# Kernel tuning notes

Hardware: AMD Instinct MI355X
Metric: run time of the kernel (lower is better)

## Reference

```python
import jax, jax.numpy as jnp
import numpy as np

D_MODEL = 1024
N_HEAD = 16
D_K = D_MODEL // N_HEAD


def setup_inputs() -> dict:
    key = jax.random.key(0)
    ks = jax.random.split(key, 9)
    s = 1.0 / np.sqrt(D_MODEL)
    return {
        "x": jax.random.normal(ks[0], (2, 2048, D_MODEL), dtype=jnp.float32),
        "Wq": jax.random.uniform(ks[1], (D_MODEL, D_MODEL), jnp.float32, -s, s),
        "bq": jax.random.uniform(ks[2], (D_MODEL,), jnp.float32, -s, s),
        "Wk": jax.random.uniform(ks[3], (D_MODEL, D_MODEL), jnp.float32, -s, s),
        "bk": jax.random.uniform(ks[4], (D_MODEL,), jnp.float32, -s, s),
        "Wv": jax.random.uniform(ks[5], (D_MODEL, D_MODEL), jnp.float32, -s, s),
        "bv": jax.random.uniform(ks[6], (D_MODEL,), jnp.float32, -s, s),
        "Wo": jax.random.uniform(ks[7], (D_MODEL, D_MODEL), jnp.float32, -s, s),
        "bo": jax.random.uniform(ks[8], (D_MODEL,), jnp.float32, -s, s),
    }


def reference(x, Wq, bq, Wk, bk, Wv, bv, Wo, bo):
    B, S, D = x.shape
    # linear projections (torch Linear: x @ W.T + b)
    q = x @ Wq.T + bq
    k = x @ Wk.T + bk
    v = x @ Wv.T + bv
    # split heads: [B, H, S, d_k]
    q = q.reshape(B, S, N_HEAD, D_K).transpose(0, 2, 1, 3)
    k = k.reshape(B, S, N_HEAD, D_K).transpose(0, 2, 1, 3)
    v = v.reshape(B, S, N_HEAD, D_K).transpose(0, 2, 1, 3)
    scores = jnp.einsum("bhqd,bhkd->bhqk", q, k) / np.sqrt(D_K).astype(jnp.float32)
    attn = jax.nn.softmax(scores, axis=-1)
    out = jnp.einsum("bhqk,bhkd->bhqd", attn, v)
    out = out.transpose(0, 2, 1, 3).reshape(B, S, D)
    return out @ Wo.T + bo
```

## Files before the change

kernel.cpp:

```cpp
#include <hip/hip_runtime.h>
#include <hip/hip_bf16.h>


typedef unsigned short u16;
typedef __attribute__((ext_vector_type(4))) unsigned short u16x4;
typedef __attribute__((ext_vector_type(8))) short short8;
typedef __attribute__((ext_vector_type(4))) float f32x4;

__device__ __forceinline__ u16 f2bf(float f) {
  __bf16 b = (__bf16)f;
  return __builtin_bit_cast(unsigned short, b);
}

__device__ __forceinline__ f32x4 mfma_bf16(short8 a, short8 b, f32x4 c) {
  return __builtin_amdgcn_mfma_f32_16x16x32_bf16(a, b, c, 0, 0, 0);
}

#define GLL16(gp, lp) __builtin_amdgcn_global_load_lds( \
    (const __attribute__((address_space(1))) void*)(gp), \
    (__attribute__((address_space(3))) void*)(lp), 16, 0, 0)

#define QSCALE 0.18033688011112042f

__global__ __launch_bounds__(256) void cast_all(
    const float* __restrict__ x,
    const float* __restrict__ wq, const float* __restrict__ wk,
    const float* __restrict__ wv, const float* __restrict__ wo,
    u16* __restrict__ xb, u16* __restrict__ wqb, u16* __restrict__ wkb,
    u16* __restrict__ wvb, u16* __restrict__ wob)
{
  const int z = blockIdx.z;
  const float* s; u16* d; int n4;
  if (z == 0)      { s = x;  d = xb;  n4 = 1048576; }
  else if (z == 1) { s = wq; d = wqb; n4 = 262144; }
  else if (z == 2) { s = wk; d = wkb; n4 = 262144; }
  else if (z == 3) { s = wv; d = wvb; n4 = 262144; }
  else             { s = wo; d = wob; n4 = 262144; }
  int i = blockIdx.x * 256 + threadIdx.x;
  if (i >= n4) return;
  float4 v = ((const float4*)s)[i];
  u16x4 o; o[0] = f2bf(v.x); o[1] = f2bf(v.y); o[2] = f2bf(v.z); o[3] = f2bf(v.w);
  ((u16x4*)d)[i] = o;
}

__global__ __launch_bounds__(512, 2) void gemm_qkv(
    const u16* __restrict__ X, const u16* __restrict__ Wqkv,
    const float* __restrict__ bq, const float* __restrict__ bk, const float* __restrict__ bv,
    u16* __restrict__ Qo, u16* __restrict__ Ko, u16* __restrict__ Vt)
{
  __shared__ u16 smem[65536];
  u16* const sA0 = smem;
  u16* const sA1 = smem + 16384;
  u16* const sB0 = smem + 32768;
  u16* const sB1 = smem + 49152;

  const int tid = threadIdx.x, lane = tid & 63, w = tid >> 6;
  const int wr = w >> 2, wcn = w & 3;
  const int rl = lane & 15, g = lane >> 4, rsw = rl & 7;

  const int bflat = blockIdx.x;
  const int xcd = bflat & 7, idx = bflat >> 3;
  const int mt = xcd * 2 + (idx & 1);
  const int nt = idx >> 1;
  const int m0 = mt * 256;
  const int z = nt >> 2;
  const int colbase = (nt & 3) * 256;

  const int lr = lane >> 3, lc = lane & 7;
  const size_t srcoff = (size_t)(w * 8 + lr) * 1024 + ((lc ^ lr) * 8);
  const u16* gaS = X    + (size_t)m0 * 1024 + srcoff;
  const u16* gbS = Wqkv + (size_t)(nt * 256) * 1024 + srcoff;

  f32x4 acc[8][4];
#pragma unroll
  for (int mf = 0; mf < 8; ++mf)
#pragma unroll
    for (int nf = 0; nf < 4; ++nf) acc[mf][nf] = (f32x4){0.f, 0.f, 0.f, 0.f};

  auto loadA = [&](const u16* buf, int mf, int kh) -> short8 {
    return *(const short8*)&buf[(wr * 128 + mf * 16 + rl) * 64 +
                                (((kh * 4 + g) ^ rsw) * 8)];
  };
  auto loadB = [&](const u16* buf, int nf, int kh) -> short8 {
    return *(const short8*)&buf[(wcn * 64 + nf * 16 + rl) * 64 +
                                (((kh * 4 + g) ^ rsw) * 8)];
  };

  auto proc_tile = [&](const u16* bufA, const u16* bufB,
                       u16* stA, u16* stB, int ts, bool doSt) {
    short8 af[4], bf[4];
    if (doSt) {
#pragma unroll
      for (int i = 0; i < 4; ++i)
        GLL16(gaS + (size_t)(i * 64) * 1024 + ts * 64, stA + (i * 64 + w * 8) * 64);
    }
#pragma unroll
    for (int nf = 0; nf < 4; ++nf) bf[nf] = loadB(bufB, nf, 0);
#pragma unroll
    for (int i = 0; i < 4; ++i) af[i] = loadA(bufA, i, 0);
    __builtin_amdgcn_s_setprio(1);
#pragma unroll
    for (int i = 0; i < 4; ++i)
#pragma unroll
      for (int nf = 0; nf < 4; ++nf)
        acc[i][nf] = mfma_bf16(af[i], bf[nf], acc[i][nf]);
    __builtin_amdgcn_s_setprio(0);
    __builtin_amdgcn_s_barrier();
    if (doSt) {
#pragma unroll
      for (int i = 0; i < 4; ++i)
        GLL16(gbS + (size_t)(i * 64) * 1024 + ts * 64, stB + (i * 64 + w * 8) * 64);
    }
#pragma unroll
    for (int i = 0; i < 4; ++i) af[i] = loadA(bufA, 4 + i, 0);
    __builtin_amdgcn_s_setprio(1);
#pragma unroll
    for (int i = 0; i < 4; ++i)
#pragma unroll
      for (int nf = 0; nf < 4; ++nf)
        acc[4 + i][nf] = mfma_bf16(af[i], bf[nf], acc[4 + i][nf]);
    __builtin_amdgcn_s_setprio(0);
    __builtin_amdgcn_s_barrier();
#pragma unroll
    for (int nf = 0; nf < 4; ++nf) bf[nf] = loadB(bufB, nf, 1);
#pragma unroll
    for (int i = 0; i < 4; ++i) af[i] = loadA(bufA, i, 1);
    __builtin_amdgcn_s_setprio(1);
#pragma unroll
    for (int i = 0; i < 4; ++i)
#pragma unroll
      for (int nf = 0; nf < 4; ++nf)
        acc[i][nf] = mfma_bf16(af[i], bf[nf], acc[i][nf]);
    __builtin_amdgcn_s_setprio(0);
    __builtin_amdgcn_s_barrier();
#pragma unroll
    for (int i = 0; i < 4; ++i) af[i] = loadA(bufA, 4 + i, 1);
    __builtin_amdgcn_s_setprio(1);
#pragma unroll
    for (int i = 0; i < 4; ++i)
#pragma unroll
      for (int nf = 0; nf < 4; ++nf)
        acc[4 + i][nf] = mfma_bf16(af[i], bf[nf], acc[4 + i][nf]);
    __builtin_amdgcn_s_setprio(0);
  };

#pragma unroll
  for (int i = 0; i < 4; ++i) {
    GLL16(gaS + (size_t)(i * 64) * 1024, sA0 + (i * 64 + w * 8) * 64);
    GLL16(gbS + (size_t)(i * 64) * 1024, sB0 + (i * 64 + w * 8) * 64);
  }
  __syncthreads();

#pragma unroll 1
  for (int tt = 0; tt < 8; ++tt) {
    proc_tile(sA0, sB0, sA1, sB1, 2 * tt + 1, true);
    __syncthreads();
    proc_tile(sA1, sB1, sA0, sB0, 2 * tt + 2, tt < 7);
    __syncthreads();
  }

  const int rg = g * 4;
  if (z < 2) {
    u16* dst = (z == 0) ? Qo : Ko;
    const float cs = (z == 0) ? QSCALE : 1.0f;
    const float* bias = (z == 0) ? bq : bk;
#pragma unroll
    for (int nf = 0; nf < 4; ++nf) {
      int col = colbase + wcn * 64 + nf * 16 + rl;
      float bb = bias[col];
#pragma unroll
      for (int mf = 0; mf < 8; ++mf) {
        int row0 = m0 + wr * 128 + mf * 16 + rg;
#pragma unroll
        for (int r = 0; r < 4; ++r)
          dst[(size_t)(row0 + r) * 1024 + col] = f2bf((acc[mf][nf][r] + bb) * cs);
      }
    }
  } else {
#pragma unroll
    for (int nf = 0; nf < 4; ++nf) {
      int col = colbase + wcn * 64 + nf * 16 + rl;
      float bb = bv[col];
#pragma unroll
      for (int mf = 0; mf < 8; ++mf) {
        int row0 = m0 + wr * 128 + mf * 16 + rg;
        int bidx = row0 >> 11, sl = row0 & 2047;
        u16x4 pk;
#pragma unroll
        for (int r = 0; r < 4; ++r) pk[r] = f2bf(acc[mf][nf][r] + bb);
        *(u16x4*)&Vt[((size_t)(bidx * 1024 + col)) * 2048 + sl] = pk;
      }
    }
  }
}

__global__ __launch_bounds__(256) void gemm_out(
    const u16* __restrict__ Ob, const u16* __restrict__ Wob,
    const float* __restrict__ bo, float* __restrict__ Out)
{
  __shared__ u16 sA[2048], sB[4096];
  const int bflat = blockIdx.x;
  const int xcd = bflat & 7, idx = bflat >> 3;
  const int m0 = (xcd * 8 + (idx & 7)) * 64;
  const int n0 = (idx >> 3) * 128;

  const int tid = threadIdx.x, lane = tid & 63, wave = tid >> 6;
  const int wr = wave >> 1, wc = wave & 1;
  const u16* ga = Ob  + (size_t)(m0 + (tid >> 2)) * 1024 + (tid & 3) * 8;
  const u16* gb = Wob + (size_t)(n0 + (tid >> 2)) * 1024 + (tid & 3) * 8;
  u16* la0 = sA + wave * 512;
  u16* lb0 = sB + wave * 512;          u16* lb1 = sB + 2048 + wave * 512;
  const int rl = lane & 15, kg = (lane >> 4) * 8, rg = (lane >> 4) * 4;

  f32x4 acc[2][4];
#pragma unroll
  for (int m = 0; m < 2; ++m)
#pragma unroll
    for (int n = 0; n < 4; ++n) acc[m][n] = (f32x4){0.f, 0.f, 0.f, 0.f};

  for (int k0 = 0; k0 < 1024; k0 += 32) {
    GLL16(ga + k0,             la0);
    GLL16(gb + k0,             lb0);
    GLL16(gb + 64 * 1024 + k0, lb1);
    __syncthreads();
    short8 af[2], bf_[4];
#pragma unroll
    for (int m = 0; m < 2; ++m) af[m]  = *(const short8*)&sA[(wr * 32 + m * 16 + rl) * 32 + kg];
#pragma unroll
    for (int n = 0; n < 4; ++n) bf_[n] = *(const short8*)&sB[(wc * 64 + n * 16 + rl) * 32 + kg];
#pragma unroll
    for (int m = 0; m < 2; ++m)
#pragma unroll
      for (int n = 0; n < 4; ++n)
        acc[m][n] = mfma_bf16(af[m], bf_[n], acc[m][n]);
    __syncthreads();
  }

#pragma unroll
  for (int n = 0; n < 4; ++n) {
    int col = n0 + wc * 64 + n * 16 + rl;
    float bb = bo[col];
#pragma unroll
    for (int m = 0; m < 2; ++m) {
      int row0 = m0 + wr * 32 + m * 16 + rg;
#pragma unroll
      for (int r = 0; r < 4; ++r)
        Out[(size_t)(row0 + r) * 1024 + col] = acc[m][n][r] + bb;
    }
  }
}

__global__ __launch_bounds__(512) void attn_fwd(
    const u16* __restrict__ Q, const u16* __restrict__ K,
    const u16* __restrict__ Vt, u16* __restrict__ O)
{
  __shared__ u16 sK[2][64][64];
  __shared__ u16 sV[2][64][64];

  const int tid = threadIdx.x, lane = tid & 63, wave = tid >> 6;
  const int rl = lane & 15, g = lane >> 4;

  const int bflat = blockIdx.x;
  const int xcd = bflat & 7, j = bflat >> 3;
  const int bh = xcd * 4 + (j >> 4);
  const int qchunk = j & 15;
  const int b = bh >> 4, h = bh & 15;
  const int qbase = qchunk * 128 + wave * 16;

  const u16* Qp = Q + (size_t)(b * 2048 + qbase) * 1024 + h * 64;
  const u16* Kp = K + (size_t)(b * 2048) * 1024 + h * 64;
  const u16* Vp = Vt + (size_t)(bh * 64) * 2048;

  short8 qf[2];
#pragma unroll
  for (int hf = 0; hf < 2; ++hf)
    qf[hf] = *(const short8*)&Qp[(size_t)rl * 1024 + hf * 32 + g * 8];

  const int keyperm = 8 * (rl >> 2) + (rl & 3);
  const int swzK8 = (((rl & 3) | (((rl >> 2) & 1) << 2))) * 8;
  const int swzV8 = (rl & 7) * 8;

  const int srow = lane >> 3;
  const int feK = (((lane & 7) ^ (srow & 3)) * 8) ^ ((wave & 1) * 32);
  const int feV = (((lane & 7) ^ srow) * 8);

  f32x4 oacc[4];
  f32x4 lacc = (f32x4){0.f, 0.f, 0.f, 0.f};
#pragma unroll
  for (int dg = 0; dg < 4; ++dg) oacc[dg] = (f32x4){0.f, 0.f, 0.f, 0.f};
  float mrun = -INFINITY;

  const short8 ONES = {0x3F80, 0x3F80, 0x3F80, 0x3F80,
                       0x3F80, 0x3F80, 0x3F80, 0x3F80};

  auto stage = [&](int nb, int kt) {
    const int grow = wave * 8 + srow;
    GLL16(Kp + (size_t)(kt + grow) * 1024 + feK, &sK[nb][wave * 8][0]);
    GLL16(Vp + (size_t)grow * 2048 + kt + feV,   &sV[nb][wave * 8][0]);
  };

  auto proc_sub = [&](int nb, int sub) {
    short8 kf[2][2];
#pragma unroll
    for (int t = 0; t < 2; ++t) {
      const int r = sub * 32 + keyperm + 4 * t;
#pragma unroll
      for (int hf = 0; hf < 2; ++hf)
        kf[t][hf] = *(const short8*)&sK[nb][r][(hf * 32 + g * 8) ^ swzK8];
    }
    short8 vf[4];
#pragma unroll
    for (int dg = 0; dg < 4; ++dg)
      vf[dg] = *(const short8*)&sV[nb][dg * 16 + rl][(sub * 32 + g * 8) ^ swzV8];

    f32x4 sc[2];
    __builtin_amdgcn_s_setprio(1);
#pragma unroll
    for (int t = 0; t < 2; ++t) {
      f32x4 a = (f32x4){0.f, 0.f, 0.f, 0.f};
      a = mfma_bf16(kf[t][0], qf[0], a);
      a = mfma_bf16(kf[t][1], qf[1], a);
      sc[t] = a;
    }
    __builtin_amdgcn_s_setprio(0);

    float p2[8];
#pragma unroll
    for (int t = 0; t < 2; ++t)
#pragma unroll
      for (int r = 0; r < 4; ++r) p2[t * 4 + r] = sc[t][r];
    float a0 = fmaxf(fmaxf(p2[0], p2[1]), p2[2]);
    float a1 = fmaxf(fmaxf(p2[3], p2[4]), p2[5]);
    float a2 = fmaxf(p2[6], p2[7]);
    float tm = fmaxf(fmaxf(a0, a1), a2);
    if (!__all(tm <= mrun + 8.0f)) {
      tm = fmaxf(tm, __shfl_xor(tm, 16));
      tm = fmaxf(tm, __shfl_xor(tm, 32));
      float mnew = fmaxf(mrun, tm);
      float sfac = __builtin_amdgcn_exp2f(mrun - mnew);
      mrun = mnew;
#pragma unroll
      for (int dg = 0; dg < 4; ++dg)
#pragma unroll
        for (int r = 0; r < 4; ++r) oacc[dg][r] *= sfac;
      lacc[0] *= sfac;
    }
    short8 pb;
#pragma unroll
    for (int j2 = 0; j2 < 8; ++j2)
      pb[j2] = (short)f2bf(__builtin_amdgcn_exp2f(p2[j2] - mrun));

    __builtin_amdgcn_s_setprio(1);
    lacc = mfma_bf16(ONES, pb, lacc);
#pragma unroll
    for (int dg = 0; dg < 4; ++dg)
      oacc[dg] = mfma_bf16(vf[dg], pb, oacc[dg]);
    __builtin_amdgcn_s_setprio(0);
  };

  stage(0, 0);
  __syncthreads();
  for (int kt = 0; kt < 2048; kt += 128) {
    stage(1, kt + 64);
    proc_sub(0, 0);
    proc_sub(0, 1);
    __syncthreads();
    if (kt + 128 < 2048) stage(0, kt + 128);
    proc_sub(1, 0);
    proc_sub(1, 1);
    __syncthreads();
  }

  float inv = 1.0f / lacc[0];
  int qrow = qbase + rl;
  u16* op = O + (size_t)(b * 2048 + qrow) * 1024 + h * 64;
#pragma unroll
  for (int dg = 0; dg < 4; ++dg) {
    u16x4 pk;
#pragma unroll
    for (int r = 0; r < 4; ++r) pk[r] = f2bf(oacc[dg][r] * inv);
    *(u16x4*)&op[dg * 16 + g * 4] = pk;
  }
}

extern "C" void kernel_launch(void* const* d_in, const int* in_sizes, int n_in,
                              void* d_out, int out_size, void* d_ws, size_t ws_size,
                              hipStream_t stream) {
  const float* x  = (const float*)d_in[0];
  const float* Wq = (const float*)d_in[1];
  const float* bq = (const float*)d_in[2];
  const float* Wk = (const float*)d_in[3];
  const float* bk = (const float*)d_in[4];
  const float* Wv = (const float*)d_in[5];
  const float* bv = (const float*)d_in[6];
  const float* Wo = (const float*)d_in[7];
  const float* bo = (const float*)d_in[8];

  char* ws = (char*)d_ws;
  const size_t MB = 1024 * 1024;
  u16* Xb  = (u16*)(ws + 0 * MB);
  u16* Wqb = (u16*)(ws + 8 * MB);
  u16* Wkb = (u16*)(ws + 10 * MB);
  u16* Wvb = (u16*)(ws + 12 * MB);
  u16* Wob = (u16*)(ws + 14 * MB);
  u16* Qb  = (u16*)(ws + 16 * MB);
  u16* Kb  = (u16*)(ws + 24 * MB);
  u16* Vtb = (u16*)(ws + 32 * MB);
  u16* Ob  = (u16*)(ws + 40 * MB);

  cast_all<<<dim3(4096, 1, 5), 256, 0, stream>>>(x, Wq, Wk, Wv, Wo,
                                                 Xb, Wqb, Wkb, Wvb, Wob);
  gemm_qkv<<<dim3(192), 512, 0, stream>>>(Xb, Wqb, bq, bk, bv, Qb, Kb, Vtb);
  attn_fwd<<<dim3(512), 512, 0, stream>>>(Qb, Kb, Vtb, Ob);
  gemm_out<<<dim3(512), 256, 0, stream>>>(Ob, Wob, bo, (float*)d_out);
}
```

Before: 110.5 us.

## Retile output projection to 256x256 double-buffered GEMM and flatten cast grid

The output projection GEMM moves from 64x128 tiles with a single LDS buffer to the 256x256 tile scheme used by the QKV GEMM. That scheme uses 512 threads, a double-buffered XOR-swizzled LDS layout, 64-wide K steps and interleaved prefetch with setprio around the MFMA blocks. The goal is more data reuse per block and hiding global load latency. The trade-off is that only 64 blocks are launched, which may leave many CUs idle on a 256-CU part. The cast kernel also drops the z-dimension grid, which removed the wasted blocks that covered the smaller weight tensors, and now writes the weights as one contiguous panel.

```diff
diff --git a/kernel.cpp b/kernel.cpp
--- a/kernel.cpp
+++ b/kernel.cpp
@@ -26,21 +26,22 @@
     const float* __restrict__ x,
     const float* __restrict__ wq, const float* __restrict__ wk,
     const float* __restrict__ wv, const float* __restrict__ wo,
-    u16* __restrict__ xb, u16* __restrict__ wqb, u16* __restrict__ wkb,
-    u16* __restrict__ wvb, u16* __restrict__ wob)
+    u16* __restrict__ xb, u16* __restrict__ wpanel)
 {
-  const int z = blockIdx.z;
-  const float* s; u16* d; int n4;
-  if (z == 0)      { s = x;  d = xb;  n4 = 1048576; }
-  else if (z == 1) { s = wq; d = wqb; n4 = 262144; }
-  else if (z == 2) { s = wk; d = wkb; n4 = 262144; }
-  else if (z == 3) { s = wv; d = wvb; n4 = 262144; }
-  else             { s = wo; d = wob; n4 = 262144; }
   int i = blockIdx.x * 256 + threadIdx.x;
-  if (i >= n4) return;
+  const float* s; u16x4* d;
+  if (i < 1048576) {
+    s = x; d = (u16x4*)xb + i;
+  } else {
+    int j = i - 1048576;
+    int w = j >> 18;
+    const float* ws4 = (w == 0) ? wq : (w == 1) ? wk : (w == 2) ? wv : wo;
+    s = ws4; d = (u16x4*)wpanel + j;
+    i = j & 262143;
+  }
   float4 v = ((const float4*)s)[i];
   u16x4 o; o[0] = f2bf(v.x); o[1] = f2bf(v.y); o[2] = f2bf(v.z); o[3] = f2bf(v.w);
-  ((u16x4*)d)[i] = o;
+  *d = o;
 }
 
 __global__ __launch_bounds__(512, 2) void gemm_qkv(
@@ -194,58 +195,130 @@
   }
 }
 
-__global__ __launch_bounds__(256) void gemm_out(
+__global__ __launch_bounds__(512, 2) void gemm_out(
     const u16* __restrict__ Ob, const u16* __restrict__ Wob,
     const float* __restrict__ bo, float* __restrict__ Out)
 {
-  __shared__ u16 sA[2048], sB[4096];
+  __shared__ u16 smem[65536];
+  u16* const sA0 = smem;
+  u16* const sA1 = smem + 16384;
+  u16* const sB0 = smem + 32768;
+  u16* const sB1 = smem + 49152;
+
+  const int tid = threadIdx.x, lane = tid & 63, w = tid >> 6;
+  const int wr = w >> 2, wcn = w & 3;
+  const int rl = lane & 15, g = lane >> 4, rsw = rl & 7;
+
   const int bflat = blockIdx.x;
   const int xcd = bflat & 7, idx = bflat >> 3;
-  const int m0 = (xcd * 8 + (idx & 7)) * 64;
-  const int n0 = (idx >> 3) * 128;
-
-  const int tid = threadIdx.x, lane = tid & 63, wave = tid >> 6;
-  const int wr = wave >> 1, wc = wave & 1;
-  const u16* ga = Ob  + (size_t)(m0 + (tid >> 2)) * 1024 + (tid & 3) * 8;
-  const u16* gb = Wob + (size_t)(n0 + (tid >> 2)) * 1024 + (tid & 3) * 8;
-  u16* la0 = sA + wave * 512;
-  u16* lb0 = sB + wave * 512;          u16* lb1 = sB + 2048 + wave * 512;
-  const int rl = lane & 15, kg = (lane >> 4) * 8, rg = (lane >> 4) * 4;
-
-  f32x4 acc[2][4];
-#pragma unroll
-  for (int m = 0; m < 2; ++m)
-#pragma unroll
-    for (int n = 0; n < 4; ++n) acc[m][n] = (f32x4){0.f, 0.f, 0.f, 0.f};
-
-  for (int k0 = 0; k0 < 1024; k0 += 32) {
-    GLL16(ga + k0,             la0);
-    GLL16(gb + k0,             lb0);
-    GLL16(gb + 64 * 1024 + k0, lb1);
-    __syncthreads();
-    short8 af[2], bf_[4];
-#pragma unroll
-    for (int m = 0; m < 2; ++m) af[m]  = *(const short8*)&sA[(wr * 32 + m * 16 + rl) * 32 + kg];
-#pragma unroll
-    for (int n = 0; n < 4; ++n) bf_[n] = *(const short8*)&sB[(wc * 64 + n * 16 + rl) * 32 + kg];
-#pragma unroll
-    for (int m = 0; m < 2; ++m)
-#pragma unroll
-      for (int n = 0; n < 4; ++n)
-        acc[m][n] = mfma_bf16(af[m], bf_[n], acc[m][n]);
-    __syncthreads();
-  }
-
-#pragma unroll
-  for (int n = 0; n < 4; ++n) {
-    int col = n0 + wc * 64 + n * 16 + rl;
+  const int mt = xcd * 2 + (idx & 1);
+  const int nt = idx >> 1;
+  const int m0 = mt * 256;
+
+  const int lr = lane >> 3, lc = lane & 7;
+  const size_t srcoff = (size_t)(w * 8 + lr) * 1024 + ((lc ^ lr) * 8);
+  const u16* gaS = Ob  + (size_t)m0 * 1024 + srcoff;
+  const u16* gbS = Wob + (size_t)(nt * 256) * 1024 + srcoff;
+
+  f32x4 acc[8][4];
+#pragma unroll
+  for (int mf = 0; mf < 8; ++mf)
+#pragma unroll
+    for (int nf = 0; nf < 4; ++nf) acc[mf][nf] = (f32x4){0.f, 0.f, 0.f, 0.f};
+
+  auto loadA = [&](const u16* buf, int mf, int kh) -> short8 {
+    return *(const short8*)&buf[(wr * 128 + mf * 16 + rl) * 64 +
+                                (((kh * 4 + g) ^ rsw) * 8)];
+  };
+  auto loadB = [&](const u16* buf, int nf, int kh) -> short8 {
+    return *(const short8*)&buf[(wcn * 64 + nf * 16 + rl) * 64 +
+                                (((kh * 4 + g) ^ rsw) * 8)];
+  };
+
+  auto proc_tile = [&](const u16* bufA, const u16* bufB,
+                       u16* stA, u16* stB, int ts, bool doSt) {
+    short8 af[4], bf[4];
+    if (doSt) {
+#pragma unroll
+      for (int i = 0; i < 4; ++i)
+        GLL16(gaS + (size_t)(i * 64) * 1024 + ts * 64, stA + (i * 64 + w * 8) * 64);
+    }
+#pragma unroll
+    for (int nf = 0; nf < 4; ++nf) bf[nf] = loadB(bufB, nf, 0);
+#pragma unroll
+    for (int i = 0; i < 4; ++i) af[i] = loadA(bufA, i, 0);
+    __builtin_amdgcn_s_setprio(1);
+#pragma unroll
+    for (int i = 0; i < 4; ++i)
+#pragma unroll
+      for (int nf = 0; nf < 4; ++nf)
+        acc[i][nf] = mfma_bf16(af[i], bf[nf], acc[i][nf]);
+    __builtin_amdgcn_s_setprio(0);
+    __builtin_amdgcn_s_barrier();
+    if (doSt) {
+#pragma unroll
+      for (int i = 0; i < 4; ++i)
+        GLL16(gbS + (size_t)(i * 64) * 1024 + ts * 64, stB + (i * 64 + w * 8) * 64);
+    }
+#pragma unroll
+    for (int i = 0; i < 4; ++i) af[i] = loadA(bufA, 4 + i, 0);
+    __builtin_amdgcn_s_setprio(1);
+#pragma unroll
+    for (int i = 0; i < 4; ++i)
+#pragma unroll
+      for (int nf = 0; nf < 4; ++nf)
+        acc[4 + i][nf] = mfma_bf16(af[i], bf[nf], acc[4 + i][nf]);
+    __builtin_amdgcn_s_setprio(0);
+    __builtin_amdgcn_s_barrier();
+#pragma unroll
+    for (int nf = 0; nf < 4; ++nf) bf[nf] = loadB(bufB, nf, 1);
+#pragma unroll
+    for (int i = 0; i < 4; ++i) af[i] = loadA(bufA, i, 1);
+    __builtin_amdgcn_s_setprio(1);
+#pragma unroll
+    for (int i = 0; i < 4; ++i)
+#pragma unroll
+      for (int nf = 0; nf < 4; ++nf)
+        acc[i][nf] = mfma_bf16(af[i], bf[nf], acc[i][nf]);
+    __builtin_amdgcn_s_setprio(0);
+    __builtin_amdgcn_s_barrier();
+#pragma unroll
+    for (int i = 0; i < 4; ++i) af[i] = loadA(bufA, 4 + i, 1);
+    __builtin_amdgcn_s_setprio(1);
+#pragma unroll
+    for (int i = 0; i < 4; ++i)
+#pragma unroll
+      for (int nf = 0; nf < 4; ++nf)
+        acc[4 + i][nf] = mfma_bf16(af[i], bf[nf], acc[4 + i][nf]);
+    __builtin_amdgcn_s_setprio(0);
+  };
+
+#pragma unroll
+  for (int i = 0; i < 4; ++i) {
+    GLL16(gaS + (size_t)(i * 64) * 1024, sA0 + (i * 64 + w * 8) * 64);
+    GLL16(gbS + (size_t)(i * 64) * 1024, sB0 + (i * 64 + w * 8) * 64);
+  }
+  __syncthreads();
+
+#pragma unroll 1
+  for (int tt = 0; tt < 8; ++tt) {
+    proc_tile(sA0, sB0, sA1, sB1, 2 * tt + 1, true);
+    __syncthreads();
+    proc_tile(sA1, sB1, sA0, sB0, 2 * tt + 2, tt < 7);
+    __syncthreads();
+  }
+
+  const int rg = g * 4;
+#pragma unroll
+  for (int nf = 0; nf < 4; ++nf) {
+    int col = nt * 256 + wcn * 64 + nf * 16 + rl;
     float bb = bo[col];
 #pragma unroll
-    for (int m = 0; m < 2; ++m) {
-      int row0 = m0 + wr * 32 + m * 16 + rg;
+    for (int mf = 0; mf < 8; ++mf) {
+      int row0 = m0 + wr * 128 + mf * 16 + rg;
 #pragma unroll
       for (int r = 0; r < 4; ++r)
-        Out[(size_t)(row0 + r) * 1024 + col] = acc[m][n][r] + bb;
+        Out[(size_t)(row0 + r) * 1024 + col] = acc[mf][nf][r] + bb;
     }
   }
 }
@@ -400,17 +473,14 @@
   const size_t MB = 1024 * 1024;
   u16* Xb  = (u16*)(ws + 0 * MB);
   u16* Wqb = (u16*)(ws + 8 * MB);
-  u16* Wkb = (u16*)(ws + 10 * MB);
-  u16* Wvb = (u16*)(ws + 12 * MB);
   u16* Wob = (u16*)(ws + 14 * MB);
   u16* Qb  = (u16*)(ws + 16 * MB);
   u16* Kb  = (u16*)(ws + 24 * MB);
   u16* Vtb = (u16*)(ws + 32 * MB);
   u16* Ob  = (u16*)(ws + 40 * MB);
 
-  cast_all<<<dim3(4096, 1, 5), 256, 0, stream>>>(x, Wq, Wk, Wv, Wo,
-                                                 Xb, Wqb, Wkb, Wvb, Wob);
+  cast_all<<<dim3(8192), 256, 0, stream>>>(x, Wq, Wk, Wv, Wo, Xb, Wqb);
   gemm_qkv<<<dim3(192), 512, 0, stream>>>(Xb, Wqb, bq, bk, bv, Qb, Kb, Vtb);
   attn_fwd<<<dim3(512), 512, 0, stream>>>(Qb, Kb, Vtb, Ob);
-  gemm_out<<<dim3(512), 256, 0, stream>>>(Ob, Wob, bo, (float*)d_out);
-}
+  gemm_out<<<dim3(64), 512, 0, stream>>>(Ob, Wob, bo, (float*)d_out);
+}
```

New measurement: 118.0 us. +6.9%, slower.
